# Kernel tuning notes

Measured on AMD Instinct MI355X. Metric: run time of the kernel, lower is better.

Reference implementation:

```python
import jax, jax.numpy as jnp
import numpy as np

B, C, P = 32, 192, 3136
EPS = 0.01


def setup_inputs() -> dict:
    key = jax.random.key(0)
    k1, k2, k3 = jax.random.split(key, 3)
    return {
        "embeddings": jax.random.normal(k1, (B, C, P), dtype=jnp.float32),
        "means": jax.random.normal(k2, (P, C), dtype=jnp.float32),
        "covariances": jax.random.normal(k3, (P, C, C), dtype=jnp.float32),
        "n": 96,
    }


def reference(embeddings, means, covariances, n):
    # embeddings: [B, C, P]; means: [P, C] (running sums); covariances: [P, C, C] (running outer-product sums)
    b = embeddings.shape[0]
    c = embeddings.shape[1]
    # Training-branch accumulation: per-patch sum of outer products over the batch,
    # expressed as one batched GEMM instead of P*B tiny torch.outer calls.
    new_means = means + jnp.einsum("bcp->pc", embeddings)
    new_covs = covariances + jnp.einsum("bcp,bdp->pcd", embeddings, embeddings)
    n_new = n + b
    # calculate_means_and_covariances(): finalize sample mean / covariance per patch.
    learned_means = new_means / n_new  # [P, C]
    learned_covs = (new_covs - n_new * jnp.einsum("pc,pd->pcd", learned_means, learned_means)) / (n_new - 1)
    learned_covs = learned_covs + EPS * jnp.eye(c, dtype=learned_covs.dtype)
    return (learned_means, learned_covs)
```

## Files before the change

### kernel.cpp

```cpp
#include <hip/hip_runtime.h>


#define BB 32
#define CC 192
#define PP 3136
#define EPSV 0.01f

__global__ __launch_bounds__(256, 3) void padim_kernel(
    const float* __restrict__ emb,
    const float* __restrict__ means,
    const float* __restrict__ covs,
    const int*   __restrict__ n_ptr,
    float* __restrict__ out_means,
    float* __restrict__ out_covs)
{
    __shared__ __align__(16) float E[BB][CC];
    __shared__ __align__(16) float m[CC];

    const int bid = blockIdx.x;
    const int p = (bid & 7) * (PP / 8) + (bid >> 3);
    const int t = threadIdx.x;

    const float n_new = (float)(n_ptr[0] + BB);
    const float inv_nnew = 1.0f / n_new;
    const float inv_nm1 = 1.0f / (n_new - 1.0f);

    #pragma unroll
    for (int k = 0; k < (BB * CC) / 256; ++k) {
        const int i = t + k * 256;
        const int b = i / CC;
        const int c = i - b * CC;
        E[b][c] = emb[(size_t)i * PP + p];
    }
    __syncthreads();

    if (t < CC) {
        float s = 0.0f;
        #pragma unroll
        for (int b = 0; b < BB; ++b) s += E[b][t];
        const float mm = (means[(size_t)p * CC + t] + s) * inv_nnew;
        m[t] = mm;
        out_means[(size_t)p * CC + t] = mm;
    }
    __syncthreads();

    const int tx = t & 15;
    const int ty = t >> 4;
    const int dbase0 = tx * 4;

    const float* __restrict__ cov_p = covs + (size_t)p * CC * CC;
    float* __restrict__ out_p = out_covs + (size_t)p * CC * CC;

    float md[12];
    *reinterpret_cast<float4*>(&md[0]) = *reinterpret_cast<const float4*>(&m[dbase0]);
    *reinterpret_cast<float4*>(&md[4]) = *reinterpret_cast<const float4*>(&m[64 + dbase0]);
    *reinterpret_cast<float4*>(&md[8]) = *reinterpret_cast<const float4*>(&m[128 + dbase0]);

    #pragma unroll
    for (int pass = 0; pass < 2; ++pass) {
        const int c0 = pass * 96 + ty * 6;

        float acc[6][12];
        #pragma unroll
        for (int i = 0; i < 6; ++i)
            #pragma unroll
            for (int j = 0; j < 12; ++j) acc[i][j] = 0.f;

        #pragma unroll 4
        for (int b = 0; b < BB; ++b) {
            float cs[6], ds[12];
            *reinterpret_cast<float4*>(&ds[0]) = *reinterpret_cast<const float4*>(&E[b][dbase0]);
            *reinterpret_cast<float4*>(&ds[4]) = *reinterpret_cast<const float4*>(&E[b][64 + dbase0]);
            *reinterpret_cast<float4*>(&ds[8]) = *reinterpret_cast<const float4*>(&E[b][128 + dbase0]);
            *reinterpret_cast<float2*>(&cs[0]) = *reinterpret_cast<const float2*>(&E[b][c0]);
            *reinterpret_cast<float2*>(&cs[2]) = *reinterpret_cast<const float2*>(&E[b][c0 + 2]);
            *reinterpret_cast<float2*>(&cs[4]) = *reinterpret_cast<const float2*>(&E[b][c0 + 4]);
            #pragma unroll
            for (int i = 0; i < 6; ++i)
                #pragma unroll
                for (int j = 0; j < 12; ++j)
                    acc[i][j] = fmaf(cs[i], ds[j], acc[i][j]);
        }

        float mc[6];
        *reinterpret_cast<float2*>(&mc[0]) = *reinterpret_cast<const float2*>(&m[c0]);
        *reinterpret_cast<float2*>(&mc[2]) = *reinterpret_cast<const float2*>(&m[c0 + 2]);
        *reinterpret_cast<float2*>(&mc[4]) = *reinterpret_cast<const float2*>(&m[c0 + 4]);

        #pragma unroll
        for (int i = 0; i < 6; ++i) {
            const int c = c0 + i;
            const size_t row = (size_t)c * CC;
            const float nmc = n_new * mc[i];
            #pragma unroll
            for (int g = 0; g < 3; ++g) {
                const int db = g * 64 + dbase0;
                const float4 cin = *reinterpret_cast<const float4*>(&cov_p[row + db]);
                float4 o;
                o.x = (cin.x + acc[i][g*4+0] - nmc * md[g*4+0]) * inv_nm1;
                o.y = (cin.y + acc[i][g*4+1] - nmc * md[g*4+1]) * inv_nm1;
                o.z = (cin.z + acc[i][g*4+2] - nmc * md[g*4+2]) * inv_nm1;
                o.w = (cin.w + acc[i][g*4+3] - nmc * md[g*4+3]) * inv_nm1;
                const int dd = c - db;
                if (dd == 0) o.x += EPSV;
                if (dd == 1) o.y += EPSV;
                if (dd == 2) o.z += EPSV;
                if (dd == 3) o.w += EPSV;
                *reinterpret_cast<float4*>(&out_p[row + db]) = o;
            }
        }
    }
}

extern "C" void kernel_launch(void* const* d_in, const int* in_sizes, int n_in,
                              void* d_out, int out_size, void* d_ws, size_t ws_size,
                              hipStream_t stream) {
    const float* emb   = (const float*)d_in[0];
    const float* means = (const float*)d_in[1];
    const float* covs  = (const float*)d_in[2];
    const int*   n_ptr = (const int*)d_in[3];

    float* out_means = (float*)d_out;
    float* out_covs  = (float*)d_out + (size_t)PP * CC;

    hipLaunchKernelGGL(padim_kernel, dim3(PP), dim3(256), 0, stream,
                       emb, means, covs, n_ptr, out_means, out_covs);
}
```

Baseline: 252.7 us.

## Pre-transpose embeddings into workspace and use nontemporal covariance stores

Adds a tiled transpose kernel that rewrites the embeddings into a per-patch contiguous layout in the workspace. The main kernel can then load each patch's 32x192 slice with coalesced float4 reads instead of strided scalar gathers. Covariance output stores become nontemporal. The cost is an extra pass that reads and writes the full embedding tensor (about 77 MB) and an added launch; if the workspace is too small, a fallback kernel runs instead.

```diff
diff --git a/kernel.cpp b/kernel.cpp
--- a/kernel.cpp
+++ b/kernel.cpp
@@ -4,40 +4,64 @@
 #define BB 32
 #define CC 192
 #define PP 3136
+#define II (BB * CC)
 #define EPSV 0.01f
 
-__global__ __launch_bounds__(256, 3) void padim_kernel(
-    const float* __restrict__ emb,
+typedef float nat_float4 __attribute__((ext_vector_type(4)));
+
+__global__ __launch_bounds__(256) void transpose_kernel(
+    const float* __restrict__ emb, float* __restrict__ Et)
+{
+    __shared__ float tile[64][65];
+    const int i0 = blockIdx.x * 64;
+    const int p0 = blockIdx.y * 64;
+    const int t = threadIdx.x;
+    const int tc = t & 63;
+    const int tr4 = t >> 6;
+
+    #pragma unroll
+    for (int k = 0; k < 16; ++k) {
+        const int r = k * 4 + tr4;
+        tile[r][tc] = emb[(size_t)(i0 + r) * PP + (p0 + tc)];
+    }
+    __syncthreads();
+    #pragma unroll
+    for (int k = 0; k < 16; ++k) {
+        const int r = k * 4 + tr4;
+        Et[(size_t)(p0 + r) * II + (i0 + tc)] = tile[tc][r];
+    }
+}
+
+__global__ __launch_bounds__(256, 3) void padim_main(
+    const float* __restrict__ Et,
     const float* __restrict__ means,
     const float* __restrict__ covs,
     const int*   __restrict__ n_ptr,
     float* __restrict__ out_means,
     float* __restrict__ out_covs)
 {
-    __shared__ __align__(16) float E[BB][CC];
+    __shared__ __align__(16) float E[II];
     __shared__ __align__(16) float m[CC];
 
-    const int bid = blockIdx.x;
-    const int p = (bid & 7) * (PP / 8) + (bid >> 3);
+    const int p = blockIdx.x;
     const int t = threadIdx.x;
 
     const float n_new = (float)(n_ptr[0] + BB);
     const float inv_nnew = 1.0f / n_new;
     const float inv_nm1 = 1.0f / (n_new - 1.0f);
 
-    #pragma unroll
-    for (int k = 0; k < (BB * CC) / 256; ++k) {
-        const int i = t + k * 256;
-        const int b = i / CC;
-        const int c = i - b * CC;
-        E[b][c] = emb[(size_t)i * PP + p];
+    {
+        const float4* __restrict__ src = reinterpret_cast<const float4*>(Et + (size_t)p * II);
+        float4* dst = reinterpret_cast<float4*>(E);
+        #pragma unroll
+        for (int k = 0; k < 6; ++k) dst[k * 256 + t] = src[k * 256 + t];
     }
     __syncthreads();
 
     if (t < CC) {
         float s = 0.0f;
         #pragma unroll
-        for (int b = 0; b < BB; ++b) s += E[b][t];
+        for (int b = 0; b < BB; ++b) s += E[b * CC + t];
         const float mm = (means[(size_t)p * CC + t] + s) * inv_nnew;
         m[t] = mm;
         out_means[(size_t)p * CC + t] = mm;
@@ -68,13 +92,14 @@
 
         #pragma unroll 4
         for (int b = 0; b < BB; ++b) {
+            const float* __restrict__ Eb = E + b * CC;
             float cs[6], ds[12];
-            *reinterpret_cast<float4*>(&ds[0]) = *reinterpret_cast<const float4*>(&E[b][dbase0]);
-            *reinterpret_cast<float4*>(&ds[4]) = *reinterpret_cast<const float4*>(&E[b][64 + dbase0]);
-            *reinterpret_cast<float4*>(&ds[8]) = *reinterpret_cast<const float4*>(&E[b][128 + dbase0]);
-            *reinterpret_cast<float2*>(&cs[0]) = *reinterpret_cast<const float2*>(&E[b][c0]);
-            *reinterpret_cast<float2*>(&cs[2]) = *reinterpret_cast<const float2*>(&E[b][c0 + 2]);
-            *reinterpret_cast<float2*>(&cs[4]) = *reinterpret_cast<const float2*>(&E[b][c0 + 4]);
+            *reinterpret_cast<float4*>(&ds[0]) = *reinterpret_cast<const float4*>(&Eb[dbase0]);
+            *reinterpret_cast<float4*>(&ds[4]) = *reinterpret_cast<const float4*>(&Eb[64 + dbase0]);
+            *reinterpret_cast<float4*>(&ds[8]) = *reinterpret_cast<const float4*>(&Eb[128 + dbase0]);
+            *reinterpret_cast<float2*>(&cs[0]) = *reinterpret_cast<const float2*>(&Eb[c0]);
+            *reinterpret_cast<float2*>(&cs[2]) = *reinterpret_cast<const float2*>(&Eb[c0 + 2]);
+            *reinterpret_cast<float2*>(&cs[4]) = *reinterpret_cast<const float2*>(&Eb[c0 + 4]);
             #pragma unroll
             for (int i = 0; i < 6; ++i)
                 #pragma unroll
@@ -87,6 +112,95 @@
         *reinterpret_cast<float2*>(&mc[2]) = *reinterpret_cast<const float2*>(&m[c0 + 2]);
         *reinterpret_cast<float2*>(&mc[4]) = *reinterpret_cast<const float2*>(&m[c0 + 4]);
 
+        #pragma unroll
+        for (int i = 0; i < 6; ++i) {
+            const int c = c0 + i;
+            const size_t row = (size_t)c * CC;
+            const float nmc = n_new * mc[i];
+            #pragma unroll
+            for (int g = 0; g < 3; ++g) {
+                const int db = g * 64 + dbase0;
+                const float4 cin = *reinterpret_cast<const float4*>(&cov_p[row + db]);
+                nat_float4 o;
+                o.x = (cin.x + acc[i][g*4+0] - nmc * md[g*4+0]) * inv_nm1;
+                o.y = (cin.y + acc[i][g*4+1] - nmc * md[g*4+1]) * inv_nm1;
+                o.z = (cin.z + acc[i][g*4+2] - nmc * md[g*4+2]) * inv_nm1;
+                o.w = (cin.w + acc[i][g*4+3] - nmc * md[g*4+3]) * inv_nm1;
+                const int dd = c - db;
+                if (dd == 0) o.x += EPSV;
+                if (dd == 1) o.y += EPSV;
+                if (dd == 2) o.z += EPSV;
+                if (dd == 3) o.w += EPSV;
+                __builtin_nontemporal_store(o, reinterpret_cast<nat_float4*>(&out_p[row + db]));
+            }
+        }
+    }
+}
+
+__global__ __launch_bounds__(256, 3) void padim_fallback(
+    const float* __restrict__ emb, const float* __restrict__ means,
+    const float* __restrict__ covs, const int* __restrict__ n_ptr,
+    float* __restrict__ out_means, float* __restrict__ out_covs)
+{
+    __shared__ __align__(16) float E[II];
+    __shared__ __align__(16) float m[CC];
+    const int bid = blockIdx.x;
+    const int p = (bid & 7) * (PP / 8) + (bid >> 3);
+    const int t = threadIdx.x;
+    const float n_new = (float)(n_ptr[0] + BB);
+    const float inv_nnew = 1.0f / n_new;
+    const float inv_nm1 = 1.0f / (n_new - 1.0f);
+    #pragma unroll
+    for (int k = 0; k < II / 256; ++k) {
+        const int i = t + k * 256;
+        E[i] = emb[(size_t)i * PP + p];
+    }
+    __syncthreads();
+    if (t < CC) {
+        float s = 0.0f;
+        #pragma unroll
+        for (int b = 0; b < BB; ++b) s += E[b * CC + t];
+        const float mm = (means[(size_t)p * CC + t] + s) * inv_nnew;
+        m[t] = mm;
+        out_means[(size_t)p * CC + t] = mm;
+    }
+    __syncthreads();
+    const int tx = t & 15, ty = t >> 4;
+    const int dbase0 = tx * 4;
+    const float* __restrict__ cov_p = covs + (size_t)p * CC * CC;
+    float* __restrict__ out_p = out_covs + (size_t)p * CC * CC;
+    float md[12];
+    *reinterpret_cast<float4*>(&md[0]) = *reinterpret_cast<const float4*>(&m[dbase0]);
+    *reinterpret_cast<float4*>(&md[4]) = *reinterpret_cast<const float4*>(&m[64 + dbase0]);
+    *reinterpret_cast<float4*>(&md[8]) = *reinterpret_cast<const float4*>(&m[128 + dbase0]);
+    #pragma unroll
+    for (int pass = 0; pass < 2; ++pass) {
+        const int c0 = pass * 96 + ty * 6;
+        float acc[6][12];
+        #pragma unroll
+        for (int i = 0; i < 6; ++i)
+            #pragma unroll
+            for (int j = 0; j < 12; ++j) acc[i][j] = 0.f;
+        #pragma unroll 4
+        for (int b = 0; b < BB; ++b) {
+            const float* __restrict__ Eb = E + b * CC;
+            float cs[6], ds[12];
+            *reinterpret_cast<float4*>(&ds[0]) = *reinterpret_cast<const float4*>(&Eb[dbase0]);
+            *reinterpret_cast<float4*>(&ds[4]) = *reinterpret_cast<const float4*>(&Eb[64 + dbase0]);
+            *reinterpret_cast<float4*>(&ds[8]) = *reinterpret_cast<const float4*>(&Eb[128 + dbase0]);
+            *reinterpret_cast<float2*>(&cs[0]) = *reinterpret_cast<const float2*>(&Eb[c0]);
+            *reinterpret_cast<float2*>(&cs[2]) = *reinterpret_cast<const float2*>(&Eb[c0 + 2]);
+            *reinterpret_cast<float2*>(&cs[4]) = *reinterpret_cast<const float2*>(&Eb[c0 + 4]);
+            #pragma unroll
+            for (int i = 0; i < 6; ++i)
+                #pragma unroll
+                for (int j = 0; j < 12; ++j)
+                    acc[i][j] = fmaf(cs[i], ds[j], acc[i][j]);
+        }
+        float mc[6];
+        *reinterpret_cast<float2*>(&mc[0]) = *reinterpret_cast<const float2*>(&m[c0]);
+        *reinterpret_cast<float2*>(&mc[2]) = *reinterpret_cast<const float2*>(&m[c0 + 2]);
+        *reinterpret_cast<float2*>(&mc[4]) = *reinterpret_cast<const float2*>(&m[c0 + 4]);
         #pragma unroll
         for (int i = 0; i < 6; ++i) {
             const int c = c0 + i;
@@ -123,6 +237,15 @@
     float* out_means = (float*)d_out;
     float* out_covs  = (float*)d_out + (size_t)PP * CC;
 
-    hipLaunchKernelGGL(padim_kernel, dim3(PP), dim3(256), 0, stream,
-                       emb, means, covs, n_ptr, out_means, out_covs);
-}
+    const size_t et_bytes = (size_t)PP * II * sizeof(float);
+    if (ws_size >= et_bytes) {
+        float* Et = (float*)d_ws;
+        hipLaunchKernelGGL(transpose_kernel, dim3(II / 64, PP / 64), dim3(256),
+                           0, stream, emb, Et);
+        hipLaunchKernelGGL(padim_main, dim3(PP), dim3(256), 0, stream,
+                           Et, means, covs, n_ptr, out_means, out_covs);
+    } else {
+        hipLaunchKernelGGL(padim_fallback, dim3(PP), dim3(256), 0, stream,
+                           emb, means, covs, n_ptr, out_means, out_covs);
+    }
+}
```

New measurement: 234.5 us. 7.2% less time.

## Pretranspose embeddings to bf16 and compute outer-product sums with MFMA

Applied to the files above, without the earlier changes.

Adds a transpose kernel that converts embeddings to bf16 in a patch-major workspace layout, then uses bf16 MFMA 16x16x32 instructions to form the per-patch Gram matrices. Work is split over two column slabs per patch, and nontemporal loads and stores are used for the covariance stream. This removes the strided per-patch gather and the scalar FMA work, at the cost of an extra kernel pass and bf16 rounding of the inputs, which lowers the precision of both the means and the covariances. A path that needs no workspace is kept as a fallback.

```diff
diff --git a/kernel.cpp b/kernel.cpp
--- a/kernel.cpp
+++ b/kernel.cpp
@@ -4,89 +4,216 @@
 #define BB 32
 #define CC 192
 #define PP 3136
+#define II (BB * CC)
 #define EPSV 0.01f
 
-__global__ __launch_bounds__(256, 3) void padim_kernel(
-    const float* __restrict__ emb,
+typedef float f32x4 __attribute__((ext_vector_type(4)));
+typedef short bf16x8 __attribute__((ext_vector_type(8)));
+
+__device__ __forceinline__ unsigned short f2bf(float f) {
+    unsigned int u = __float_as_uint(f);
+    u += 0x7fffu + ((u >> 16) & 1u);
+    return (unsigned short)(u >> 16);
+}
+__device__ __forceinline__ float bflo(unsigned int u) { return __uint_as_float(u << 16); }
+__device__ __forceinline__ float bfhi(unsigned int u) { return __uint_as_float(u & 0xffff0000u); }
+
+__global__ __launch_bounds__(256) void transpose_bf16(
+    const float* __restrict__ emb, unsigned short* __restrict__ Et)
+{
+    __shared__ unsigned short tile[512 * 34];
+    const int c0 = blockIdx.x * 16;
+    const int p0 = blockIdx.y * 32;
+    const int t = threadIdx.x;
+    const int tc = t & 31;
+    const int rg = t >> 5;
+
+    #pragma unroll 8
+    for (int k = 0; k < 64; ++k) {
+        const int r = k * 8 + rg;
+        const int b = r & 31;
+        const int cl = r >> 5;
+        const float v = __builtin_nontemporal_load(
+            &emb[(size_t)(b * CC + c0 + cl) * PP + (p0 + tc)]);
+        tile[r * 34 + tc] = f2bf(v);
+    }
+    __syncthreads();
+
+    const int pl = t >> 3;
+    unsigned short* dst = Et + (size_t)(p0 + pl) * II + c0 * 32;
+    #pragma unroll
+    for (int w = 0; w < 8; ++w) {
+        const int q = w * 8 + (t & 7);
+        const int rbase = (q >> 2) * 32 + (q & 3) * 8;
+        unsigned int dw[4];
+        #pragma unroll
+        for (int j = 0; j < 4; ++j) {
+            const unsigned int lo = tile[(rbase + 2 * j) * 34 + pl];
+            const unsigned int hi = tile[(rbase + 2 * j + 1) * 34 + pl];
+            dw[j] = lo | (hi << 16);
+        }
+        uint4 val; val.x = dw[0]; val.y = dw[1]; val.z = dw[2]; val.w = dw[3];
+        *reinterpret_cast<uint4*>(dst + q * 8) = val;
+    }
+}
+
+__global__ __launch_bounds__(256, 3) void padim_mfma(
+    const unsigned short* __restrict__ Et,
     const float* __restrict__ means,
     const float* __restrict__ covs,
     const int*   __restrict__ n_ptr,
     float* __restrict__ out_means,
     float* __restrict__ out_covs)
 {
-    __shared__ __align__(16) float E[BB][CC];
+    __shared__ float m_lds[CC];
+
+    const int bid = blockIdx.x;
+    const int u = (bid & 7) * (PP * 2 / 8) + (bid >> 3);
+    const int slab = u & 1;
+    const int p = u >> 1;
+
+    const int t = threadIdx.x;
+    const int lane = t & 63;
+    const int w = t >> 6;
+    const int l15 = lane & 15;
+    const int l4  = lane >> 4;
+
+    const float n_new = (float)(n_ptr[0] + BB);
+    const float inv_nnew = 1.0f / n_new;
+    const float inv_nm1 = 1.0f / (n_new - 1.0f);
+
+    const unsigned short* __restrict__ Erow = Et + (size_t)p * II;
+
+    bf16x8 Af[3], Bf[6];
+    #pragma unroll
+    for (int dt = 0; dt < 3; ++dt) {
+        const int rA = (3 * w + dt) * 16 + l15;
+        Af[dt] = *reinterpret_cast<const bf16x8*>(Erow + rA * 32 + l4 * 8);
+    }
+    #pragma unroll
+    for (int ct = 0; ct < 6; ++ct) {
+        const int rB = (slab * 6 + ct) * 16 + l15;
+        Bf[ct] = *reinterpret_cast<const bf16x8*>(Erow + rB * 32 + l4 * 8);
+    }
+
+    if (t < CC) {
+        const uint4* rp = reinterpret_cast<const uint4*>(Erow + t * 32);
+        float s = 0.f;
+        #pragma unroll
+        for (int q = 0; q < 4; ++q) {
+            const uint4 v = rp[q];
+            s += bflo(v.x) + bfhi(v.x) + bflo(v.y) + bfhi(v.y)
+               + bflo(v.z) + bfhi(v.z) + bflo(v.w) + bfhi(v.w);
+        }
+        const float mm = (means[(size_t)p * CC + t] + s) * inv_nnew;
+        m_lds[t] = mm;
+        if (slab == 0) out_means[(size_t)p * CC + t] = mm;
+    }
+    __syncthreads();
+
+    f32x4 acc[3][6];
+    #pragma unroll
+    for (int dt = 0; dt < 3; ++dt)
+        #pragma unroll
+        for (int ct = 0; ct < 6; ++ct)
+            acc[dt][ct] = (f32x4){0.f, 0.f, 0.f, 0.f};
+
+    #pragma unroll
+    for (int ct = 0; ct < 6; ++ct)
+        #pragma unroll
+        for (int dt = 0; dt < 3; ++dt)
+            acc[dt][ct] = __builtin_amdgcn_mfma_f32_16x16x32_bf16(
+                Af[dt], Bf[ct], acc[dt][ct], 0, 0, 0);
+
+    const float* __restrict__ cov_p = covs + (size_t)p * CC * CC;
+    float* __restrict__ out_p = out_covs + (size_t)p * CC * CC;
+
+    #pragma unroll
+    for (int dt = 0; dt < 3; ++dt) {
+        const int d0 = (3 * w + dt) * 16 + l4 * 4;
+        const f32x4 md = *reinterpret_cast<const f32x4*>(&m_lds[d0]);
+        #pragma unroll
+        for (int ct = 0; ct < 6; ++ct) {
+            const int c = (slab * 6 + ct) * 16 + l15;
+            const float nmc = n_new * m_lds[c];
+            const size_t off = (size_t)c * CC + d0;
+            const f32x4 cin = __builtin_nontemporal_load(
+                reinterpret_cast<const f32x4*>(cov_p + off));
+            f32x4 o = (cin + acc[dt][ct] - nmc * md) * inv_nm1;
+            const int dd = c - d0;
+            o.x += (dd == 0) ? EPSV : 0.f;
+            o.y += (dd == 1) ? EPSV : 0.f;
+            o.z += (dd == 2) ? EPSV : 0.f;
+            o.w += (dd == 3) ? EPSV : 0.f;
+            __builtin_nontemporal_store(o, reinterpret_cast<f32x4*>(out_p + off));
+        }
+    }
+}
+
+__global__ __launch_bounds__(256, 3) void padim_fallback(
+    const float* __restrict__ emb, const float* __restrict__ means,
+    const float* __restrict__ covs, const int* __restrict__ n_ptr,
+    float* __restrict__ out_means, float* __restrict__ out_covs)
+{
+    __shared__ __align__(16) float E[II];
     __shared__ __align__(16) float m[CC];
-
     const int bid = blockIdx.x;
     const int p = (bid & 7) * (PP / 8) + (bid >> 3);
     const int t = threadIdx.x;
-
     const float n_new = (float)(n_ptr[0] + BB);
     const float inv_nnew = 1.0f / n_new;
     const float inv_nm1 = 1.0f / (n_new - 1.0f);
-
-    #pragma unroll
-    for (int k = 0; k < (BB * CC) / 256; ++k) {
+    #pragma unroll
+    for (int k = 0; k < II / 256; ++k) {
         const int i = t + k * 256;
-        const int b = i / CC;
-        const int c = i - b * CC;
-        E[b][c] = emb[(size_t)i * PP + p];
-    }
-    __syncthreads();
-
+        E[i] = emb[(size_t)i * PP + p];
+    }
+    __syncthreads();
     if (t < CC) {
         float s = 0.0f;
         #pragma unroll
-        for (int b = 0; b < BB; ++b) s += E[b][t];
+        for (int b = 0; b < BB; ++b) s += E[b * CC + t];
         const float mm = (means[(size_t)p * CC + t] + s) * inv_nnew;
         m[t] = mm;
         out_means[(size_t)p * CC + t] = mm;
     }
     __syncthreads();
-
-    const int tx = t & 15;
-    const int ty = t >> 4;
+    const int tx = t & 15, ty = t >> 4;
     const int dbase0 = tx * 4;
-
     const float* __restrict__ cov_p = covs + (size_t)p * CC * CC;
     float* __restrict__ out_p = out_covs + (size_t)p * CC * CC;
-
     float md[12];
     *reinterpret_cast<float4*>(&md[0]) = *reinterpret_cast<const float4*>(&m[dbase0]);
     *reinterpret_cast<float4*>(&md[4]) = *reinterpret_cast<const float4*>(&m[64 + dbase0]);
     *reinterpret_cast<float4*>(&md[8]) = *reinterpret_cast<const float4*>(&m[128 + dbase0]);
-
     #pragma unroll
     for (int pass = 0; pass < 2; ++pass) {
         const int c0 = pass * 96 + ty * 6;
-
         float acc[6][12];
         #pragma unroll
         for (int i = 0; i < 6; ++i)
             #pragma unroll
             for (int j = 0; j < 12; ++j) acc[i][j] = 0.f;
-
         #pragma unroll 4
         for (int b = 0; b < BB; ++b) {
+            const float* __restrict__ Eb = E + b * CC;
             float cs[6], ds[12];
-            *reinterpret_cast<float4*>(&ds[0]) = *reinterpret_cast<const float4*>(&E[b][dbase0]);
-            *reinterpret_cast<float4*>(&ds[4]) = *reinterpret_cast<const float4*>(&E[b][64 + dbase0]);
-            *reinterpret_cast<float4*>(&ds[8]) = *reinterpret_cast<const float4*>(&E[b][128 + dbase0]);
-            *reinterpret_cast<float2*>(&cs[0]) = *reinterpret_cast<const float2*>(&E[b][c0]);
-            *reinterpret_cast<float2*>(&cs[2]) = *reinterpret_cast<const float2*>(&E[b][c0 + 2]);
-            *reinterpret_cast<float2*>(&cs[4]) = *reinterpret_cast<const float2*>(&E[b][c0 + 4]);
+            *reinterpret_cast<float4*>(&ds[0]) = *reinterpret_cast<const float4*>(&Eb[dbase0]);
+            *reinterpret_cast<float4*>(&ds[4]) = *reinterpret_cast<const float4*>(&Eb[64 + dbase0]);
+            *reinterpret_cast<float4*>(&ds[8]) = *reinterpret_cast<const float4*>(&Eb[128 + dbase0]);
+            *reinterpret_cast<float2*>(&cs[0]) = *reinterpret_cast<const float2*>(&Eb[c0]);
+            *reinterpret_cast<float2*>(&cs[2]) = *reinterpret_cast<const float2*>(&Eb[c0 + 2]);
+            *reinterpret_cast<float2*>(&cs[4]) = *reinterpret_cast<const float2*>(&Eb[c0 + 4]);
             #pragma unroll
             for (int i = 0; i < 6; ++i)
                 #pragma unroll
                 for (int j = 0; j < 12; ++j)
                     acc[i][j] = fmaf(cs[i], ds[j], acc[i][j]);
         }
-
         float mc[6];
         *reinterpret_cast<float2*>(&mc[0]) = *reinterpret_cast<const float2*>(&m[c0]);
         *reinterpret_cast<float2*>(&mc[2]) = *reinterpret_cast<const float2*>(&m[c0 + 2]);
         *reinterpret_cast<float2*>(&mc[4]) = *reinterpret_cast<const float2*>(&m[c0 + 4]);
-
         #pragma unroll
         for (int i = 0; i < 6; ++i) {
             const int c = c0 + i;
@@ -123,6 +250,15 @@
     float* out_means = (float*)d_out;
     float* out_covs  = (float*)d_out + (size_t)PP * CC;
 
-    hipLaunchKernelGGL(padim_kernel, dim3(PP), dim3(256), 0, stream,
-                       emb, means, covs, n_ptr, out_means, out_covs);
-}
+    const size_t et_bytes = (size_t)PP * II * sizeof(unsigned short);
+    if (ws_size >= et_bytes) {
+        unsigned short* Et = (unsigned short*)d_ws;
+        hipLaunchKernelGGL(transpose_bf16, dim3(CC / 16, PP / 32), dim3(256),
+                           0, stream, emb, Et);
+        hipLaunchKernelGGL(padim_mfma, dim3(PP * 2), dim3(256), 0, stream,
+                           Et, means, covs, n_ptr, out_means, out_covs);
+    } else {
+        hipLaunchKernelGGL(padim_fallback, dim3(PP), dim3(256), 0, stream,
+                           emb, means, covs, n_ptr, out_means, out_covs);
+    }
+}
```

Result: slower. 306.9 us (+21.4%).

## Process two patches per block with bf16-packed embeddings and nontemporal cov I/O

Applied to the files above, without the earlier changes.

Each block now handles two adjacent patches, loading the embeddings as float2 and packing both patches' values as bf16 pairs into one shared array. The mean sums and the outer-product GEMM read the bf16 halves back out. Covariance reads and writes switch to nontemporal loads and stores, the grid is halved, and launch bounds are raised to 4 waves. The goal is better-coalesced embedding loads and less shared-memory and cache pressure on this bandwidth-bound kernel. The cost is precision: rounding embeddings to bf16 puts error into the means and covariances that can exceed tolerance.

```diff
diff --git a/kernel.cpp b/kernel.cpp
--- a/kernel.cpp
+++ b/kernel.cpp
@@ -4,9 +4,20 @@
 #define BB 32
 #define CC 192
 #define PP 3136
+#define II (BB * CC)
 #define EPSV 0.01f
 
-__global__ __launch_bounds__(256, 3) void padim_kernel(
+typedef float nat_float4 __attribute__((ext_vector_type(4)));
+
+__device__ __forceinline__ unsigned short f2bf(float f) {
+    unsigned int u = __float_as_uint(f);
+    u += 0x7fffu + ((u >> 16) & 1u);
+    return (unsigned short)(u >> 16);
+}
+__device__ __forceinline__ float exlo(unsigned int u) { return __uint_as_float(u << 16); }
+__device__ __forceinline__ float exhi(unsigned int u) { return __uint_as_float(u & 0xffff0000u); }
+
+__global__ __launch_bounds__(256, 4) void padim_fused(
     const float* __restrict__ emb,
     const float* __restrict__ means,
     const float* __restrict__ covs,
@@ -14,33 +25,41 @@
     float* __restrict__ out_means,
     float* __restrict__ out_covs)
 {
-    __shared__ __align__(16) float E[BB][CC];
-    __shared__ __align__(16) float m[CC];
+    __shared__ unsigned int EI[II];
+    __shared__ __align__(16) float m2[2][CC];
 
     const int bid = blockIdx.x;
-    const int p = (bid & 7) * (PP / 8) + (bid >> 3);
+    const int sw = (bid & 7) * (PP / 2 / 8) + (bid >> 3);
+    const int p0 = sw * 2;
+
     const int t = threadIdx.x;
-
     const float n_new = (float)(n_ptr[0] + BB);
     const float inv_nnew = 1.0f / n_new;
     const float inv_nm1 = 1.0f / (n_new - 1.0f);
 
     #pragma unroll
-    for (int k = 0; k < (BB * CC) / 256; ++k) {
-        const int i = t + k * 256;
-        const int b = i / CC;
-        const int c = i - b * CC;
-        E[b][c] = emb[(size_t)i * PP + p];
+    for (int k = 0; k < II / 256; ++k) {
+        const int i = k * 256 + t;
+        const float2 v = *reinterpret_cast<const float2*>(&emb[(size_t)i * PP + p0]);
+        EI[i] = (unsigned int)f2bf(v.x) | ((unsigned int)f2bf(v.y) << 16);
     }
     __syncthreads();
 
     if (t < CC) {
-        float s = 0.0f;
+        float s0 = 0.f, s1 = 0.f;
         #pragma unroll
-        for (int b = 0; b < BB; ++b) s += E[b][t];
-        const float mm = (means[(size_t)p * CC + t] + s) * inv_nnew;
-        m[t] = mm;
-        out_means[(size_t)p * CC + t] = mm;
+        for (int b = 0; b < BB; ++b) {
+            const unsigned int u = EI[b * CC + t];
+            s0 += exlo(u);
+            s1 += exhi(u);
+        }
+        const size_t i0 = (size_t)p0 * CC + t;
+        const float mm0 = (means[i0] + s0) * inv_nnew;
+        const float mm1 = (means[i0 + CC] + s1) * inv_nnew;
+        m2[0][t] = mm0;
+        m2[1][t] = mm1;
+        out_means[i0] = mm0;
+        out_means[i0 + CC] = mm1;
     }
     __syncthreads();
 
@@ -48,65 +67,84 @@
     const int ty = t >> 4;
     const int dbase0 = tx * 4;
 
-    const float* __restrict__ cov_p = covs + (size_t)p * CC * CC;
-    float* __restrict__ out_p = out_covs + (size_t)p * CC * CC;
+    #pragma unroll
+    for (int j = 0; j < 2; ++j) {
+        const float* __restrict__ cov_p = covs + (size_t)(p0 + j) * CC * CC;
+        float* __restrict__ out_p = out_covs + (size_t)(p0 + j) * CC * CC;
+        const float* __restrict__ mj = &m2[j][0];
 
-    float md[12];
-    *reinterpret_cast<float4*>(&md[0]) = *reinterpret_cast<const float4*>(&m[dbase0]);
-    *reinterpret_cast<float4*>(&md[4]) = *reinterpret_cast<const float4*>(&m[64 + dbase0]);
-    *reinterpret_cast<float4*>(&md[8]) = *reinterpret_cast<const float4*>(&m[128 + dbase0]);
+        float md[12];
+        *reinterpret_cast<float4*>(&md[0]) = *reinterpret_cast<const float4*>(&mj[dbase0]);
+        *reinterpret_cast<float4*>(&md[4]) = *reinterpret_cast<const float4*>(&mj[64 + dbase0]);
+        *reinterpret_cast<float4*>(&md[8]) = *reinterpret_cast<const float4*>(&mj[128 + dbase0]);
 
-    #pragma unroll
-    for (int pass = 0; pass < 2; ++pass) {
-        const int c0 = pass * 96 + ty * 6;
+        #pragma unroll 1
+        for (int pass = 0; pass < 2; ++pass) {
+            const int c0 = pass * 96 + ty * 6;
 
-        float acc[6][12];
-        #pragma unroll
-        for (int i = 0; i < 6; ++i)
-            #pragma unroll
-            for (int j = 0; j < 12; ++j) acc[i][j] = 0.f;
-
-        #pragma unroll 4
-        for (int b = 0; b < BB; ++b) {
-            float cs[6], ds[12];
-            *reinterpret_cast<float4*>(&ds[0]) = *reinterpret_cast<const float4*>(&E[b][dbase0]);
-            *reinterpret_cast<float4*>(&ds[4]) = *reinterpret_cast<const float4*>(&E[b][64 + dbase0]);
-            *reinterpret_cast<float4*>(&ds[8]) = *reinterpret_cast<const float4*>(&E[b][128 + dbase0]);
-            *reinterpret_cast<float2*>(&cs[0]) = *reinterpret_cast<const float2*>(&E[b][c0]);
-            *reinterpret_cast<float2*>(&cs[2]) = *reinterpret_cast<const float2*>(&E[b][c0 + 2]);
-            *reinterpret_cast<float2*>(&cs[4]) = *reinterpret_cast<const float2*>(&E[b][c0 + 4]);
+            float acc[6][12];
             #pragma unroll
             for (int i = 0; i < 6; ++i)
                 #pragma unroll
-                for (int j = 0; j < 12; ++j)
-                    acc[i][j] = fmaf(cs[i], ds[j], acc[i][j]);
-        }
+                for (int jj = 0; jj < 12; ++jj) acc[i][jj] = 0.f;
 
-        float mc[6];
-        *reinterpret_cast<float2*>(&mc[0]) = *reinterpret_cast<const float2*>(&m[c0]);
-        *reinterpret_cast<float2*>(&mc[2]) = *reinterpret_cast<const float2*>(&m[c0 + 2]);
-        *reinterpret_cast<float2*>(&mc[4]) = *reinterpret_cast<const float2*>(&m[c0 + 4]);
+            #pragma unroll 4
+            for (int b = 0; b < BB; ++b) {
+                const unsigned int* __restrict__ Eb = &EI[b * CC];
+                const uint4 d0 = *reinterpret_cast<const uint4*>(&Eb[dbase0]);
+                const uint4 d1 = *reinterpret_cast<const uint4*>(&Eb[64 + dbase0]);
+                const uint4 d2 = *reinterpret_cast<const uint4*>(&Eb[128 + dbase0]);
+                const uint2 cA = *reinterpret_cast<const uint2*>(&Eb[c0]);
+                const uint2 cB = *reinterpret_cast<const uint2*>(&Eb[c0 + 2]);
+                const uint2 cC = *reinterpret_cast<const uint2*>(&Eb[c0 + 4]);
+                float ds[12], cs[6];
+                if (j == 0) {
+                    ds[0] = exlo(d0.x); ds[1] = exlo(d0.y); ds[2]  = exlo(d0.z); ds[3]  = exlo(d0.w);
+                    ds[4] = exlo(d1.x); ds[5] = exlo(d1.y); ds[6]  = exlo(d1.z); ds[7]  = exlo(d1.w);
+                    ds[8] = exlo(d2.x); ds[9] = exlo(d2.y); ds[10] = exlo(d2.z); ds[11] = exlo(d2.w);
+                    cs[0] = exlo(cA.x); cs[1] = exlo(cA.y); cs[2]  = exlo(cB.x);
+                    cs[3] = exlo(cB.y); cs[4] = exlo(cC.x); cs[5]  = exlo(cC.y);
+                } else {
+                    ds[0] = exhi(d0.x); ds[1] = exhi(d0.y); ds[2]  = exhi(d0.z); ds[3]  = exhi(d0.w);
+                    ds[4] = exhi(d1.x); ds[5] = exhi(d1.y); ds[6]  = exhi(d1.z); ds[7]  = exhi(d1.w);
+                    ds[8] = exhi(d2.x); ds[9] = exhi(d2.y); ds[10] = exhi(d2.z); ds[11] = exhi(d2.w);
+                    cs[0] = exhi(cA.x); cs[1] = exhi(cA.y); cs[2]  = exhi(cB.x);
+                    cs[3] = exhi(cB.y); cs[4] = exhi(cC.x); cs[5]  = exhi(cC.y);
+                }
+                #pragma unroll
+                for (int i = 0; i < 6; ++i)
+                    #pragma unroll
+                    for (int jj = 0; jj < 12; ++jj)
+                        acc[i][jj] = fmaf(cs[i], ds[jj], acc[i][jj]);
+            }
 
-        #pragma unroll
-        for (int i = 0; i < 6; ++i) {
-            const int c = c0 + i;
-            const size_t row = (size_t)c * CC;
-            const float nmc = n_new * mc[i];
+            float mc[6];
+            *reinterpret_cast<float2*>(&mc[0]) = *reinterpret_cast<const float2*>(&mj[c0]);
+            *reinterpret_cast<float2*>(&mc[2]) = *reinterpret_cast<const float2*>(&mj[c0 + 2]);
+            *reinterpret_cast<float2*>(&mc[4]) = *reinterpret_cast<const float2*>(&mj[c0 + 4]);
+
             #pragma unroll
-            for (int g = 0; g < 3; ++g) {
-                const int db = g * 64 + dbase0;
-                const float4 cin = *reinterpret_cast<const float4*>(&cov_p[row + db]);
-                float4 o;
-                o.x = (cin.x + acc[i][g*4+0] - nmc * md[g*4+0]) * inv_nm1;
-                o.y = (cin.y + acc[i][g*4+1] - nmc * md[g*4+1]) * inv_nm1;
-                o.z = (cin.z + acc[i][g*4+2] - nmc * md[g*4+2]) * inv_nm1;
-                o.w = (cin.w + acc[i][g*4+3] - nmc * md[g*4+3]) * inv_nm1;
-                const int dd = c - db;
-                if (dd == 0) o.x += EPSV;
-                if (dd == 1) o.y += EPSV;
-                if (dd == 2) o.z += EPSV;
-                if (dd == 3) o.w += EPSV;
-                *reinterpret_cast<float4*>(&out_p[row + db]) = o;
+            for (int i = 0; i < 6; ++i) {
+                const int c = c0 + i;
+                const size_t row = (size_t)c * CC;
+                const float nmc = n_new * mc[i];
+                #pragma unroll
+                for (int g = 0; g < 3; ++g) {
+                    const int db = g * 64 + dbase0;
+                    const nat_float4 cin = __builtin_nontemporal_load(
+                        reinterpret_cast<const nat_float4*>(&cov_p[row + db]));
+                    nat_float4 o;
+                    o.x = (cin.x + acc[i][g*4+0] - nmc * md[g*4+0]) * inv_nm1;
+                    o.y = (cin.y + acc[i][g*4+1] - nmc * md[g*4+1]) * inv_nm1;
+                    o.z = (cin.z + acc[i][g*4+2] - nmc * md[g*4+2]) * inv_nm1;
+                    o.w = (cin.w + acc[i][g*4+3] - nmc * md[g*4+3]) * inv_nm1;
+                    const int dd = c - db;
+                    if (dd == 0) o.x += EPSV;
+                    if (dd == 1) o.y += EPSV;
+                    if (dd == 2) o.z += EPSV;
+                    if (dd == 3) o.w += EPSV;
+                    __builtin_nontemporal_store(o, reinterpret_cast<nat_float4*>(&out_p[row + db]));
+                }
             }
         }
     }
@@ -123,6 +161,6 @@
     float* out_means = (float*)d_out;
     float* out_covs  = (float*)d_out + (size_t)PP * CC;
 
-    hipLaunchKernelGGL(padim_kernel, dim3(PP), dim3(256), 0, stream,
+    hipLaunchKernelGGL(padim_fused, dim3(PP / 2), dim3(256), 0, stream,
                        emb, means, covs, n_ptr, out_means, out_covs);
 }
```

After: 276.3 us. +9.3%, slower.
